# Optimization experiments

Hardware: AMD Instinct MI355X
Metric: run time of the kernel (lower is better)

The kernel has to match this reference:

```python
import jax, jax.numpy as jnp
import numpy as np

B, N, H, W = 2, 65536, 256, 256
FEA, OUT, CMP, MAX_PT = 8, 512, 32, 64
EPS = 1e-5


def _xavier(key, fan_in, fan_out):
    scale = np.sqrt(2.0 / (fan_in + fan_out)).astype(np.float32)
    return jax.random.normal(key, (fan_in, fan_out), dtype=jnp.float32) * scale


def setup_inputs() -> dict:
    key = jax.random.key(0)
    ks = jax.random.split(key, 8)
    pt_fea = jax.random.normal(ks[0], (B, N, FEA), dtype=jnp.float32)
    xy_ind = jax.random.randint(ks[1], (B, N, 2), 0, H, dtype=jnp.int32)
    return {
        "pt_fea": pt_fea,
        "bn0_g": jnp.ones((FEA,), jnp.float32), "bn0_b": jnp.zeros((FEA,), jnp.float32),
        "W1": _xavier(ks[2], FEA, 64),
        "bn1_g": jnp.ones((64,), jnp.float32), "bn1_b": jnp.zeros((64,), jnp.float32),
        "W2": _xavier(ks[3], 64, 128),
        "bn2_g": jnp.ones((128,), jnp.float32), "bn2_b": jnp.zeros((128,), jnp.float32),
        "W3": _xavier(ks[4], 128, 256),
        "bn3_g": jnp.ones((256,), jnp.float32), "bn3_b": jnp.zeros((256,), jnp.float32),
        "W4": _xavier(ks[5], 256, OUT),
        "Wc": _xavier(ks[6], OUT, CMP),
        "xy_ind": xy_ind,
    }


def _forward(pt_fea, bn0_g, bn0_b, W1, bn1_g, bn1_b, W2, bn2_g, bn2_b,
             W3, bn3_g, bn3_b, W4, Wc, xy_ind):
    Bc, Nc, Fc = pt_fea.shape
    P = Bc * Nc
    feats = pt_fea.reshape(P, Fc)
    batch_id = jnp.repeat(jnp.arange(Bc, dtype=jnp.int32), Nc)
    xy = xy_ind.reshape(P, 2)
    keys = batch_id * (H * W) + xy[:, 0] * W + xy[:, 1]  # linearized voxel id

    # random shuffle of points (torch.randperm)
    perm = jax.random.permutation(jax.random.key(42), P)
    feats = feats[perm]
    keys = keys[perm]

    # rank of each point within its voxel, in shuffled order
    # (== grp_range_torch(unq_cnt)[argsort(argsort(unq_inv))])
    order = jnp.argsort(keys)  # stable
    sk = keys[order]
    pos = jnp.arange(P)
    new_grp = jnp.concatenate([jnp.array([True]), sk[1:] != sk[:-1]])
    grp_start = jax.lax.cummax(jnp.where(new_grp, pos, 0))
    rank = jnp.zeros(P, jnp.int32).at[order].set((pos - grp_start).astype(jnp.int32))
    mask = rank < MAX_PT  # keep at most MAX_PT points per voxel

    # PPmodel: BN -> Lin -> BN -> ReLU x3 -> Lin, BN stats over kept points only
    m = mask[:, None].astype(feats.dtype)
    cnt = jnp.sum(m)

    def bn(x, g, b):
        mu = jnp.sum(x * m, axis=0) / cnt
        var = jnp.sum(jnp.square(x - mu) * m, axis=0) / cnt  # biased var
        return (x - mu) * jax.lax.rsqrt(var + EPS) * g + b

    x = bn(feats, bn0_g, bn0_b)
    x = jax.nn.relu(bn(x @ W1, bn1_g, bn1_b))
    x = jax.nn.relu(bn(x @ W2, bn2_g, bn2_b))
    x = jax.nn.relu(bn(x @ W3, bn3_g, bn3_b))
    x = x @ W4  # [P, OUT]

    # scatter_max segment reduction into dense voxel grid
    NEG = jnp.finfo(x.dtype).min
    x = jnp.where(mask[:, None], x, NEG)
    S = Bc * H * W
    pooled = jax.ops.segment_max(x, keys, num_segments=S)
    occupied = jax.ops.segment_sum(jnp.ones(P, x.dtype), keys, num_segments=S) > 0
    pooled = jnp.where(occupied[:, None], pooled, 0.0)

    comp = jax.nn.relu(pooled @ Wc)  # fea_compression
    comp = jnp.where(occupied[:, None], comp, 0.0)  # empty voxels stay zero
    out = comp.reshape(Bc, H, W, CMP).transpose(0, 3, 1, 2)  # [B, C, H, W]
    return out


def reference(pt_fea, bn0_g, bn0_b, W1, bn1_g, bn1_b, W2, bn2_g, bn2_b,
              W3, bn3_g, bn3_b, W4, Wc, xy_ind):
    return _forward(pt_fea, bn0_g, bn0_b, W1, bn1_g, bn1_b, W2, bn2_g, bn2_b,
                    W3, bn3_g, bn3_b, W4, Wc, xy_ind)
```

## Files before the change

kernel.cpp:

```cpp
#include <hip/hip_runtime.h>
#include <cstdint>
#include <cstddef>


#define P_TOT  131072
#define HWSZ   65536
#define WGRID  256
#define S_TOT  131072
#define EPS    1e-5f
#define CNTF   131072.0f

#define OFF_Y3    0ull
#define OFF_Y1    67108864ull
#define OFF_Y2    100663296ull
#define OFF_POOL  67108864ull
#define OFF_CNT   201326592ull
#define OFF_ST    201850880ull
#define OFF_OFFS  201916416ull
#define OFF_CUR   202440704ull
#define OFF_BSUM  202964992ull
#define OFF_PIDF  202969088ull
#define OFF_SEND  203493376ull
#define OFF_SKEY  204017664ull
#define OFF_W3F   204541952ull
#define OFF_W4F   204607488ull
#define OFF_WCF   204869632ull
#define OFF_W2F   204902400ull
#define OFF_SCSH  204918784ull

typedef __attribute__((ext_vector_type(8)))  short bf16x8;
typedef __attribute__((ext_vector_type(16))) float f32x16;

__device__ __forceinline__ unsigned f2bf(float f) {
    unsigned u = __float_as_uint(f);
    return (u + 0x7FFFu + ((u >> 16) & 1u)) >> 16;
}
__device__ __forceinline__ float bf2f(unsigned h) {
    return __uint_as_float(h << 16);
}

__global__ __launch_bounds__(256) void k_zero(uint4* __restrict__ p, int n_u4) {
    int i = blockIdx.x * blockDim.x + threadIdx.x;
    if (i < n_u4) p[i] = make_uint4(0u, 0u, 0u, 0u);
}

__global__ __launch_bounds__(256) void k_prepw(
    const float* __restrict__ W2, const float* __restrict__ W3,
    const float* __restrict__ W4, const float* __restrict__ Wc,
    uint4* __restrict__ W2F, uint4* __restrict__ W3F,
    uint4* __restrict__ W4F, uint4* __restrict__ WcF)
{
    int gw = (blockIdx.x * 256 + threadIdx.x) >> 6;
    int l = threadIdx.x & 63;
    const float* W; uint4* dst; int M, mt, ks, fi;
    if (gw < 64)       { fi = gw;       W = W3; dst = W3F; M = 256; mt = fi >> 3; ks = fi & 7;  }
    else if (gw < 320) { fi = gw - 64;  W = W4; dst = W4F; M = 512; mt = fi >> 4; ks = fi & 15; }
    else if (gw < 352) { fi = gw - 320; W = Wc; dst = WcF; M = 32;  mt = 0;      ks = fi;      }
    else               { fi = gw - 352; W = W2; dst = W2F; M = 128; mt = fi >> 2; ks = fi & 3;  }
    int m = mt * 32 + (l & 31);
    int k0 = ks * 16 + (l >> 5) * 8;
    unsigned p[4];
    #pragma unroll
    for (int jj = 0; jj < 4; ++jj) {
        unsigned lo = f2bf(W[(size_t)(k0 + 2*jj)     * M + m]);
        unsigned hi = f2bf(W[(size_t)(k0 + 2*jj + 1) * M + m]);
        p[jj] = lo | (hi << 16);
    }
    dst[(size_t)fi * 64 + l] = make_uint4(p[0], p[1], p[2], p[3]);
}

__global__ __launch_bounds__(256) void k_bnprep(
    const float* __restrict__ st, const float* __restrict__ g,
    const float* __restrict__ b, float* __restrict__ sc,
    float* __restrict__ sh, int nch)
{
    int c = blockIdx.x * 256 + threadIdx.x;
    if (c >= nch) return;
    float mu = st[c * 16] * (1.0f / CNTF);
    float var = st[(nch + c) * 16] * (1.0f / CNTF) - mu * mu;
    float rs = rsqrtf(var + EPS);
    float s = rs * g[c];
    sc[c] = s;
    sh[c] = b[c] - mu * s;
}

__global__ __launch_bounds__(256) void k_fold(
    unsigned short* __restrict__ y, const float* __restrict__ sc,
    const float* __restrict__ sh, int nch, int n_u4)
{
    int i = blockIdx.x * 256 + threadIdx.x;
    if (i >= n_u4) return;
    int ch0 = (i * 8) & (nch - 1);
    float4 s0 = *(const float4*)(sc + ch0), s1 = *(const float4*)(sc + ch0 + 4);
    float4 h0 = *(const float4*)(sh + ch0), h1 = *(const float4*)(sh + ch0 + 4);
    float scv[8] = {s0.x,s0.y,s0.z,s0.w,s1.x,s1.y,s1.z,s1.w};
    float shv[8] = {h0.x,h0.y,h0.z,h0.w,h1.x,h1.y,h1.z,h1.w};
    uint4 e = ((const uint4*)y)[i];
    unsigned eu[4] = {e.x, e.y, e.z, e.w};
    unsigned ou[4];
    #pragma unroll
    for (int jj = 0; jj < 4; ++jj) {
        float x0 = fmaxf(fmaf(bf2f(eu[jj] & 0xFFFFu), scv[2*jj],   shv[2*jj]),   0.f);
        float x1 = fmaxf(fmaf(bf2f(eu[jj] >> 16),     scv[2*jj+1], shv[2*jj+1]), 0.f);
        ou[jj] = f2bf(x0) | (f2bf(x1) << 16);
    }
    ((uint4*)y)[i] = make_uint4(ou[0], ou[1], ou[2], ou[3]);
}

__global__ __launch_bounds__(256) void k_stats0(
    const float* __restrict__ pt, const int* __restrict__ xy,
    float* __restrict__ st0, unsigned* __restrict__ counts)
{
    __shared__ float part[4][16];
    const int tid = threadIdx.x;
    const int p = blockIdx.x * 256 + tid;
    const float4* f4 = (const float4*)(pt + (size_t)p * 8);
    float4 a = f4[0], b = f4[1];
    float v[8] = {a.x,a.y,a.z,a.w,b.x,b.y,b.z,b.w};
    int key = (p >> 16) * HWSZ + xy[2*p] * WGRID + xy[2*p + 1];
    atomicAdd(&counts[key], 1u);
    float s[8], q[8];
    #pragma unroll
    for (int k = 0; k < 8; ++k) { s[k] = v[k]; q[k] = v[k]*v[k]; }
    #pragma unroll
    for (int k = 0; k < 8; ++k) {
        #pragma unroll
        for (int off = 32; off > 0; off >>= 1) {
            s[k] += __shfl_down(s[k], off);
            q[k] += __shfl_down(q[k], off);
        }
    }
    if ((tid & 63) == 0) {
        int w = tid >> 6;
        #pragma unroll
        for (int k = 0; k < 8; ++k) { part[w][k] = s[k]; part[w][8 + k] = q[k]; }
    }
    __syncthreads();
    if (tid < 16) {
        float t = part[0][tid] + part[1][tid] + part[2][tid] + part[3][tid];
        atomicAdd(&st0[tid * 16], t);
    }
}

__global__ __launch_bounds__(256) void k_lin1(
    const float* __restrict__ pt, const float* __restrict__ g0,
    const float* __restrict__ b0, const float* __restrict__ W1,
    const float* __restrict__ st0, float* __restrict__ y1,
    float* __restrict__ st1)
{
    __shared__ float x0s[64 * 8];
    __shared__ float w1s[8 * 64];
    __shared__ float sc0s[8], sh0s[8];
    __shared__ float red[256];
    const int tid = threadIdx.x;

    if (tid < 8) {
        float mu = st0[tid * 16] * (1.0f / CNTF);
        float var = st0[(8 + tid) * 16] * (1.0f / CNTF) - mu * mu;
        float rs = rsqrtf(var + EPS);
        sc0s[tid] = rs * g0[tid];
        sh0s[tid] = b0[tid] - mu * rs * g0[tid];
    }
    if (tid < 128) ((float4*)w1s)[tid] = ((const float4*)W1)[tid];
    const int c = tid & 63;
    const int psub = tid >> 6;
    float ssum = 0.f, ssq = 0.f;
    for (int t = 0; t < 4; ++t) {
        const int pbase = blockIdx.x * 256 + t * 64;
        __syncthreads();
        if (tid < 128) {
            float4 f = ((const float4*)(pt + (size_t)pbase * 8))[tid];
            int cc = (tid & 1) * 4;
            f.x = fmaf(f.x, sc0s[cc + 0], sh0s[cc + 0]);
            f.y = fmaf(f.y, sc0s[cc + 1], sh0s[cc + 1]);
            f.z = fmaf(f.z, sc0s[cc + 2], sh0s[cc + 2]);
            f.w = fmaf(f.w, sc0s[cc + 3], sh0s[cc + 3]);
            ((float4*)x0s)[tid] = f;
        }
        __syncthreads();
        #pragma unroll
        for (int i = 0; i < 16; ++i) {
            int pl = psub * 16 + i;
            float acc = 0.f;
            #pragma unroll
            for (int k = 0; k < 8; ++k)
                acc = fmaf(x0s[pl * 8 + k], w1s[k * 64 + c], acc);
            y1[(size_t)(pbase + pl) * 64 + c] = acc;
            ssum += acc; ssq += acc * acc;
        }
    }
    red[tid] = ssum; __syncthreads();
    if (tid < 64) atomicAdd(&st1[tid * 16],
        red[tid] + red[tid+64] + red[tid+128] + red[tid+192]);
    __syncthreads();
    red[tid] = ssq; __syncthreads();
    if (tid < 64) atomicAdd(&st1[(64 + tid) * 16],
        red[tid] + red[tid+64] + red[tid+128] + red[tid+192]);
}

__global__ __launch_bounds__(256) void k_scan1(
    const unsigned* __restrict__ counts, unsigned* __restrict__ bsum)
{
    __shared__ unsigned sh[256];
    int t = threadIdx.x;
    sh[t] = counts[blockIdx.x * 256 + t];
    __syncthreads();
    for (int d = 128; d > 0; d >>= 1) {
        if (t < d) sh[t] += sh[t + d];
        __syncthreads();
    }
    if (t == 0) bsum[blockIdx.x] = sh[0];
}

__global__ __launch_bounds__(256) void k_scan2(
    const unsigned* __restrict__ bsum, unsigned* __restrict__ boff)
{
    __shared__ unsigned sh[256];
    int t = threadIdx.x;
    unsigned a = bsum[2*t], b = bsum[2*t+1];
    unsigned s = a + b;
    sh[t] = s; __syncthreads();
    for (int d = 1; d < 256; d <<= 1) {
        unsigned u = (t >= d) ? sh[t-d] : 0u;
        __syncthreads();
        sh[t] += u;
        __syncthreads();
    }
    unsigned excl = sh[t] - s;
    boff[2*t]   = excl;
    boff[2*t+1] = excl + a;
}

__global__ __launch_bounds__(256) void k_scan3(
    const unsigned* __restrict__ counts, const unsigned* __restrict__ boff,
    unsigned* __restrict__ offs)
{
    __shared__ unsigned sh[256];
    int t = threadIdx.x, b = blockIdx.x;
    unsigned v = counts[b*256 + t];
    sh[t] = v; __syncthreads();
    for (int d = 1; d < 256; d <<= 1) {
        unsigned u = (t >= d) ? sh[t-d] : 0u;
        __syncthreads();
        sh[t] += u;
        __syncthreads();
    }
    offs[b*256 + t] = boff[b] + sh[t] - v;
}

__global__ __launch_bounds__(256) void k_fill(
    const int* __restrict__ xy, const unsigned* __restrict__ offs,
    const unsigned* __restrict__ counts, unsigned* __restrict__ cur,
    unsigned* __restrict__ pidf, unsigned* __restrict__ send,
    unsigned* __restrict__ skey)
{
    int p = blockIdx.x * 256 + threadIdx.x;
    int key = (p >> 16) * HWSZ + xy[2*p] * WGRID + xy[2*p + 1];
    unsigned o = offs[key];
    unsigned r = atomicAdd(&cur[key], 1u);
    unsigned slot = o + r;
    pidf[slot] = (unsigned)p | (r == 0 ? 0x80000000u : 0u);
    send[slot] = o + counts[key];
    skey[slot] = (unsigned)key;
}

__global__ __launch_bounds__(256, 2) void k_lin2(
    const float* __restrict__ y1, const float* __restrict__ g1,
    const float* __restrict__ b1, const uint4* __restrict__ W2F,
    const float* __restrict__ st1, unsigned short* __restrict__ y2,
    float* __restrict__ st2)
{
    __shared__ uint4 w2s[1024];
    __shared__ float sc1s[64], sh1s[64];
    const int tid = threadIdx.x, l = tid & 63, w = tid >> 6;
    if (tid < 64) {
        float mu = st1[tid * 16] * (1.0f / CNTF);
        float var = st1[(64 + tid) * 16] * (1.0f / CNTF) - mu * mu;
        float rs = rsqrtf(var + EPS);
        sc1s[tid] = rs * g1[tid];
        sh1s[tid] = b1[tid] - mu * rs * g1[tid];
    }
    #pragma unroll
    for (int r = 0; r < 4; ++r) w2s[r * 256 + tid] = W2F[r * 256 + tid];
    __syncthreads();
    const int n = l & 31, q = l >> 5;
    float s_acc[16], q_acc[16];
    #pragma unroll
    for (int r = 0; r < 16; ++r) { s_acc[r] = 0.f; q_acc[r] = 0.f; }

    for (int t = 0; t < 8; ++t) {
        const int p = (blockIdx.x * 8 + t) * 32 + n;
        const float* yrow = y1 + (size_t)p * 64 + q * 8;
        bf16x8 Bf[4];
        #pragma unroll
        for (int ks = 0; ks < 4; ++ks) {
            float4 v0 = *(const float4*)(yrow + ks * 16);
            float4 v1 = *(const float4*)(yrow + ks * 16 + 4);
            int k0 = ks * 16 + q * 8;
            float e[8] = {v0.x,v0.y,v0.z,v0.w,v1.x,v1.y,v1.z,v1.w};
            union { bf16x8 v; unsigned u[4]; } cv;
            #pragma unroll
            for (int jj = 0; jj < 4; ++jj) {
                float a0 = fmaxf(fmaf(e[2*jj],   sc1s[k0+2*jj],   sh1s[k0+2*jj]),   0.f);
                float a1 = fmaxf(fmaf(e[2*jj+1], sc1s[k0+2*jj+1], sh1s[k0+2*jj+1]), 0.f);
                cv.u[jj] = f2bf(a0) | (f2bf(a1) << 16);
            }
            Bf[ks] = cv.v;
        }
        f32x16 acc;
        #pragma unroll
        for (int r = 0; r < 16; ++r) acc[r] = 0.f;
        #pragma unroll
        for (int ks = 0; ks < 4; ++ks) {
            union { uint4 u; bf16x8 v; } av;
            av.u = w2s[(w * 4 + ks) * 64 + l];
            acc = __builtin_amdgcn_mfma_f32_32x32x16_bf16(av.v, Bf[ks], acc, 0, 0, 0);
        }
        #pragma unroll
        for (int g = 0; g < 4; ++g) {
            int ch0 = w * 32 + 8 * g + 4 * q;
            ushort4 pk;
            pk.x = (unsigned short)f2bf(acc[4*g+0]);
            pk.y = (unsigned short)f2bf(acc[4*g+1]);
            pk.z = (unsigned short)f2bf(acc[4*g+2]);
            pk.w = (unsigned short)f2bf(acc[4*g+3]);
            *(ushort4*)(y2 + (size_t)p * 128 + ch0) = pk;
        }
        #pragma unroll
        for (int r = 0; r < 16; ++r) { s_acc[r] += acc[r]; q_acc[r] += acc[r]*acc[r]; }
    }
    #pragma unroll
    for (int r = 0; r < 16; ++r) {
        float s = s_acc[r], sq = q_acc[r];
        #pragma unroll
        for (int off = 16; off > 0; off >>= 1) {
            s  += __shfl_xor(s, off);
            sq += __shfl_xor(sq, off);
        }
        if ((l & 31) == 0) {
            int ch = w * 32 + (r & 3) + 8 * (r >> 2) + 4 * q;
            atomicAdd(&st2[ch * 16], s);
            atomicAdd(&st2[(128 + ch) * 16], sq);
        }
    }
}

__global__ __launch_bounds__(256, 2) void k_lin3(
    const unsigned short* __restrict__ y2f, const uint4* __restrict__ W3F,
    unsigned short* __restrict__ y3, float* __restrict__ st3)
{
    __shared__ uint4 w3s[4096];
    const int tid = threadIdx.x, l = tid & 63, w = tid >> 6;
    #pragma unroll
    for (int r = 0; r < 16; ++r) w3s[r * 256 + tid] = W3F[r * 256 + tid];
    __syncthreads();
    const int n = l & 31, q = l >> 5;
    float s_acc[32], q_acc[32];
    #pragma unroll
    for (int r = 0; r < 32; ++r) { s_acc[r] = 0.f; q_acc[r] = 0.f; }

    for (int t = 0; t < 8; ++t) {
        const int p = (blockIdx.x * 8 + t) * 32 + n;
        const unsigned short* yrow = y2f + (size_t)p * 128 + q * 8;
        bf16x8 Bf[8];
        #pragma unroll
        for (int ks = 0; ks < 8; ++ks) {
            union { uint4 u; bf16x8 v; } bv;
            bv.u = *(const uint4*)(yrow + ks * 16);
            Bf[ks] = bv.v;
        }
        f32x16 acc[2];
        #pragma unroll
        for (int i = 0; i < 2; ++i)
            #pragma unroll
            for (int r = 0; r < 16; ++r) acc[i][r] = 0.f;
        #pragma unroll
        for (int ks = 0; ks < 8; ++ks) {
            #pragma unroll
            for (int i = 0; i < 2; ++i) {
                union { uint4 u; bf16x8 v; } av;
                av.u = w3s[((w * 2 + i) * 8 + ks) * 64 + l];
                acc[i] = __builtin_amdgcn_mfma_f32_32x32x16_bf16(av.v, Bf[ks], acc[i], 0, 0, 0);
            }
        }
        #pragma unroll
        for (int i = 0; i < 2; ++i) {
            #pragma unroll
            for (int g = 0; g < 4; ++g) {
                int ch0 = (w * 2 + i) * 32 + 8 * g + 4 * q;
                ushort4 pk;
                pk.x = (unsigned short)f2bf(acc[i][4*g+0]);
                pk.y = (unsigned short)f2bf(acc[i][4*g+1]);
                pk.z = (unsigned short)f2bf(acc[i][4*g+2]);
                pk.w = (unsigned short)f2bf(acc[i][4*g+3]);
                *(ushort4*)(y3 + (size_t)p * 256 + ch0) = pk;
            }
            #pragma unroll
            for (int r = 0; r < 16; ++r) {
                s_acc[i*16+r] += acc[i][r];
                q_acc[i*16+r] += acc[i][r] * acc[i][r];
            }
        }
    }
    #pragma unroll
    for (int i = 0; i < 2; ++i)
        #pragma unroll
        for (int r = 0; r < 16; ++r) {
            float s = s_acc[i*16+r], sq = q_acc[i*16+r];
            #pragma unroll
            for (int off = 16; off > 0; off >>= 1) {
                s  += __shfl_xor(s, off);
                sq += __shfl_xor(sq, off);
            }
            if ((l & 31) == 0) {
                int ch = (w * 2 + i) * 32 + (r & 3) + 8 * (r >> 2) + 4 * q;
                atomicAdd(&st3[ch * 16], s);
                atomicAdd(&st3[(256 + ch) * 16], sq);
            }
        }
}

__global__ __launch_bounds__(256, 2) void k_smax(
    const unsigned short* __restrict__ y3f, const uint4* __restrict__ W4F,
    const unsigned* __restrict__ pidf, const unsigned* __restrict__ send,
    const unsigned* __restrict__ skey, unsigned short* __restrict__ pooled)
{
    __shared__ float s0c_s[4 * 256];
    const int tid = threadIdx.x, l = tid & 63, w = tid >> 6;
    const int wg = blockIdx.x;
    const int q = l >> 5;

    #pragma unroll
    for (int sub = 0; sub < 4; ++sub) s0c_s[sub * 256 + tid] = -3.4e38f;

    #pragma unroll 1
    for (int t = 8; t >= 0; --t) {
        const int p0 = (wg * 8 + t) * 32;
        const int pos = p0 + (l & 31);
        const int sp = pos < P_TOT ? pos : P_TOT - 1;
        const unsigned pf = pidf[sp];
        const unsigned e_l = send[sp];
        const unsigned key_l = skey[sp];
        const unsigned cmask =
            (unsigned)__ballot((unsigned)(pos + 1) < e_l);
        const unsigned fmask =
            (unsigned)__ballot((pf & 0x80000000u) != 0u);
        const unsigned short* row =
            y3f + (size_t)(pf & 0x7FFFFFFFu) * 256 + q * 8;
        uint4 Xf[16];
        #pragma unroll
        for (int ks = 0; ks < 16; ++ks)
            Xf[ks] = *(const uint4*)(row + ks * 16);

        #pragma unroll 1
        for (int sub = 0; sub < 4; ++sub) {
            const int nt = sub * 4 + w;
            f32x16 acc;
            #pragma unroll
            for (int r = 0; r < 16; ++r) acc[r] = 0.f;
            #pragma unroll
            for (int ks = 0; ks < 16; ++ks) {
                union { uint4 u; bf16x8 v; } xv, wv;
                xv.u = Xf[ks];
                wv.u = W4F[(size_t)(nt * 16 + ks) * 64 + l];
                acc = __builtin_amdgcn_mfma_f32_32x32x16_bf16(xv.v, wv.v, acc, 0, 0, 0);
            }
            float v[32];
            #pragma unroll
            for (int r = 0; r < 16; ++r) {
                int base = (r & 3) + 8 * (r >> 2);
                float o = __shfl_xor(acc[r], 32);
                v[base]     = q ? o : acc[r];
                v[base + 4] = q ? acc[r] : o;
            }
            if ((cmask >> 31) & 1)
                v[31] = fmaxf(v[31], s0c_s[sub * 256 + tid]);
            #pragma unroll
            for (int m = 30; m >= 0; --m)
                if ((cmask >> m) & 1) v[m] = fmaxf(v[m], v[m + 1]);
            s0c_s[sub * 256 + tid] = v[0];
            if (t < 8) {
                #pragma unroll
                for (int m = 0; m < 32; ++m) {
                    if ((fmask >> m) & 1) {
                        unsigned km = (unsigned)
                            __builtin_amdgcn_readlane((int)key_l, m);
                        if ((m >> 4) == q)
                            pooled[(size_t)km * 512 + nt * 32 + (l & 31)] =
                                (unsigned short)f2bf(v[m]);
                    }
                }
            }
        }
    }
}

__global__ __launch_bounds__(256, 4) void k_out(
    const unsigned short* __restrict__ pooled, const unsigned* __restrict__ counts,
    const uint4* __restrict__ WcF, float* __restrict__ out)
{
    __shared__ uint4 wcs[2048];
    const int tid = threadIdx.x, l = tid & 63, w = tid >> 6;
    const int sbase = blockIdx.x * 128;
    #pragma unroll
    for (int r = 0; r < 8; ++r) wcs[r * 256 + tid] = WcF[r * 256 + tid];
    __syncthreads();
    const int n = l & 31, q = l >> 5;
    const int s = sbase + w * 32 + n;
    const bool occ = counts[s] > 0;
    const unsigned short* prow =
        pooled + (occ ? (size_t)s * 512 : (size_t)0) + q * 8;
    f32x16 acc;
    #pragma unroll
    for (int r = 0; r < 16; ++r) acc[r] = 0.f;

    for (int ks = 0; ks < 32; ++ks) {
        union { uint4 u; bf16x8 v; } bv;
        bv.u = *(const uint4*)(prow + ks * 16);
        union { uint4 u; bf16x8 v; } av;
        av.u = wcs[ks * 64 + l];
        acc = __builtin_amdgcn_mfma_f32_32x32x16_bf16(av.v, bv.v, acc, 0, 0, 0);
    }
    const int b = s >> 16, hw = s & 65535;
    #pragma unroll
    for (int r = 0; r < 16; ++r) {
        int ch = (r & 3) + 8 * (r >> 2) + 4 * q;
        float x = occ ? fmaxf(acc[r], 0.f) : 0.f;
        out[(size_t)b * (32 * HWSZ) + (size_t)ch * HWSZ + hw] = x;
    }
}

extern "C" void kernel_launch(void* const* d_in, const int* in_sizes, int n_in,
                              void* d_out, int out_size, void* d_ws, size_t ws_size,
                              hipStream_t stream) {
    const float* pt = (const float*)d_in[0];
    const float* g0 = (const float*)d_in[1];
    const float* b0 = (const float*)d_in[2];
    const float* W1 = (const float*)d_in[3];
    const float* g1 = (const float*)d_in[4];
    const float* b1 = (const float*)d_in[5];
    const float* W2 = (const float*)d_in[6];
    const float* g2 = (const float*)d_in[7];
    const float* b2 = (const float*)d_in[8];
    const float* W3 = (const float*)d_in[9];
    const float* g3 = (const float*)d_in[10];
    const float* b3 = (const float*)d_in[11];
    const float* W4 = (const float*)d_in[12];
    const float* Wc = (const float*)d_in[13];
    const int*   xy = (const int*)d_in[14];
    float* out = (float*)d_out;

    char* ws = (char*)d_ws;
    unsigned short* y3     = (unsigned short*)(ws + OFF_Y3);
    float*          y1     = (float*)(ws + OFF_Y1);
    unsigned short* y2     = (unsigned short*)(ws + OFF_Y2);
    unsigned short* pool16 = (unsigned short*)(ws + OFF_POOL);
    unsigned*       counts = (unsigned*)(ws + OFF_CNT);
    float*          st     = (float*)(ws + OFF_ST);
    unsigned*       offs   = (unsigned*)(ws + OFF_OFFS);
    unsigned*       cur    = (unsigned*)(ws + OFF_CUR);
    unsigned*       bsum   = (unsigned*)(ws + OFF_BSUM);
    unsigned*       pidf   = (unsigned*)(ws + OFF_PIDF);
    unsigned*       send   = (unsigned*)(ws + OFF_SEND);
    unsigned*       skey   = (unsigned*)(ws + OFF_SKEY);
    uint4* W3F = (uint4*)(ws + OFF_W3F);
    uint4* W4F = (uint4*)(ws + OFF_W4F);
    uint4* WcF = (uint4*)(ws + OFF_WCF);
    uint4* W2F = (uint4*)(ws + OFF_W2F);
    float* scsh = (float*)(ws + OFF_SCSH);
    float* sc2 = scsh;       float* sh2 = scsh + 128;
    float* sc3 = scsh + 256; float* sh3 = scsh + 512;
    float* st0 = st;
    float* st1 = st + 256;
    float* st2 = st + 2304;
    float* st3 = st + 6400;

    k_zero<<<400, 256, 0, stream>>>((uint4*)(ws + OFF_CNT), 102400);
    k_prepw<<<92, 256, 0, stream>>>(W2, W3, W4, Wc, W2F, W3F, W4F, WcF);

    k_stats0<<<512, 256, 0, stream>>>(pt, xy, st0, counts);
    k_scan1<<<512, 256, 0, stream>>>(counts, bsum);
    k_scan2<<<1,   256, 0, stream>>>(bsum, bsum + 512);
    k_scan3<<<512, 256, 0, stream>>>(counts, bsum + 512, offs);
    k_fill<<<512, 256, 0, stream>>>(xy, offs, counts, cur, pidf, send, skey);

    k_lin1<<<512, 256, 0, stream>>>(pt, g0, b0, W1, st0, y1, st1);
    k_lin2<<<512, 256, 0, stream>>>(y1, g1, b1, W2F, st1, y2, st2);
    k_bnprep<<<1, 256, 0, stream>>>(st2, g2, b2, sc2, sh2, 128);
    k_fold<<<8192, 256, 0, stream>>>(y2, sc2, sh2, 128, 2097152);
    k_lin3<<<512, 256, 0, stream>>>(y2, W3F, y3, st3);
    k_bnprep<<<1, 256, 0, stream>>>(st3, g3, b3, sc3, sh3, 256);
    k_fold<<<16384, 256, 0, stream>>>(y3, sc3, sh3, 256, 4194304);

    k_smax<<<512, 256, 0, stream>>>(y3, W4F, pidf, send, skey, pool16);
    k_out<<<S_TOT / 128, 256, 0, stream>>>(pool16, counts, WcF, out);
}
```

Measured before the change: 441.1 us.

## Fuse layer-2 BN/ReLU into lin3 loads and double smax grid

Removes the separate bnprep and fold kernels for layer 2. k_lin3 now computes the BN scale and shift from the accumulated statistics into shared memory, then applies BN and ReLU to the raw y2 values as it loads them into MFMA operands. This saves a full read and write pass over y2 and two launches, at the cost of extra ALU work per load. Separately, k_smax now gives each workgroup 4 tiles instead of 8 and launches 1024 workgroups, trading more overlap-tile recompute for more parallelism.

```diff
diff --git a/kernel.cpp b/kernel.cpp
--- a/kernel.cpp
+++ b/kernel.cpp
@@ -346,11 +346,21 @@
 }
 
 __global__ __launch_bounds__(256, 2) void k_lin3(
-    const unsigned short* __restrict__ y2f, const uint4* __restrict__ W3F,
-    unsigned short* __restrict__ y3, float* __restrict__ st3)
+    const unsigned short* __restrict__ y2raw, const float* __restrict__ g2,
+    const float* __restrict__ b2, const uint4* __restrict__ W3F,
+    const float* __restrict__ st2, unsigned short* __restrict__ y3,
+    float* __restrict__ st3)
 {
     __shared__ uint4 w3s[4096];
+    __shared__ float sc2s[128], sh2s[128];
     const int tid = threadIdx.x, l = tid & 63, w = tid >> 6;
+    if (tid < 128) {
+        float mu = st2[tid * 16] * (1.0f / CNTF);
+        float var = st2[(128 + tid) * 16] * (1.0f / CNTF) - mu * mu;
+        float rs = rsqrtf(var + EPS);
+        sc2s[tid] = rs * g2[tid];
+        sh2s[tid] = b2[tid] - mu * rs * g2[tid];
+    }
     #pragma unroll
     for (int r = 0; r < 16; ++r) w3s[r * 256 + tid] = W3F[r * 256 + tid];
     __syncthreads();
@@ -361,13 +371,23 @@
 
     for (int t = 0; t < 8; ++t) {
         const int p = (blockIdx.x * 8 + t) * 32 + n;
-        const unsigned short* yrow = y2f + (size_t)p * 128 + q * 8;
+        const unsigned short* yrow = y2raw + (size_t)p * 128 + q * 8;
         bf16x8 Bf[8];
         #pragma unroll
         for (int ks = 0; ks < 8; ++ks) {
-            union { uint4 u; bf16x8 v; } bv;
-            bv.u = *(const uint4*)(yrow + ks * 16);
-            Bf[ks] = bv.v;
+            uint4 e = *(const uint4*)(yrow + ks * 16);
+            int k0 = ks * 16 + q * 8;
+            unsigned eu[4] = {e.x, e.y, e.z, e.w};
+            union { bf16x8 v; unsigned u[4]; } cv;
+            #pragma unroll
+            for (int jj = 0; jj < 4; ++jj) {
+                float a0 = fmaxf(fmaf(bf2f(eu[jj] & 0xFFFFu),
+                                      sc2s[k0+2*jj],   sh2s[k0+2*jj]),   0.f);
+                float a1 = fmaxf(fmaf(bf2f(eu[jj] >> 16),
+                                      sc2s[k0+2*jj+1], sh2s[k0+2*jj+1]), 0.f);
+                cv.u[jj] = f2bf(a0) | (f2bf(a1) << 16);
+            }
+            Bf[ks] = cv.v;
         }
         f32x16 acc[2];
         #pragma unroll
@@ -434,8 +454,8 @@
     for (int sub = 0; sub < 4; ++sub) s0c_s[sub * 256 + tid] = -3.4e38f;
 
     #pragma unroll 1
-    for (int t = 8; t >= 0; --t) {
-        const int p0 = (wg * 8 + t) * 32;
+    for (int t = 4; t >= 0; --t) {
+        const int p0 = (wg * 4 + t) * 32;
         const int pos = p0 + (l & 31);
         const int sp = pos < P_TOT ? pos : P_TOT - 1;
         const unsigned pf = pidf[sp];
@@ -479,7 +499,7 @@
             for (int m = 30; m >= 0; --m)
                 if ((cmask >> m) & 1) v[m] = fmaxf(v[m], v[m + 1]);
             s0c_s[sub * 256 + tid] = v[0];
-            if (t < 8) {
+            if (t < 4) {
                 #pragma unroll
                 for (int m = 0; m < 32; ++m) {
                     if ((fmask >> m) & 1) {
@@ -568,8 +588,7 @@
     uint4* WcF = (uint4*)(ws + OFF_WCF);
     uint4* W2F = (uint4*)(ws + OFF_W2F);
     float* scsh = (float*)(ws + OFF_SCSH);
-    float* sc2 = scsh;       float* sh2 = scsh + 128;
-    float* sc3 = scsh + 256; float* sh3 = scsh + 512;
+    float* sc3 = scsh;       float* sh3 = scsh + 256;
     float* st0 = st;
     float* st1 = st + 256;
     float* st2 = st + 2304;
@@ -586,12 +605,10 @@
 
     k_lin1<<<512, 256, 0, stream>>>(pt, g0, b0, W1, st0, y1, st1);
     k_lin2<<<512, 256, 0, stream>>>(y1, g1, b1, W2F, st1, y2, st2);
-    k_bnprep<<<1, 256, 0, stream>>>(st2, g2, b2, sc2, sh2, 128);
-    k_fold<<<8192, 256, 0, stream>>>(y2, sc2, sh2, 128, 2097152);
-    k_lin3<<<512, 256, 0, stream>>>(y2, W3F, y3, st3);
+    k_lin3<<<512, 256, 0, stream>>>(y2, g2, b2, W3F, st2, y3, st3);
     k_bnprep<<<1, 256, 0, stream>>>(st3, g3, b3, sc3, sh3, 256);
     k_fold<<<16384, 256, 0, stream>>>(y3, sc3, sh3, 256, 4194304);
 
-    k_smax<<<512, 256, 0, stream>>>(y3, W4F, pidf, send, skey, pool16);
+    k_smax<<<1024, 256, 0, stream>>>(y3, W4F, pidf, send, skey, pool16);
     k_out<<<S_TOT / 128, 256, 0, stream>>>(pool16, counts, WcF, out);
 }
```

Result: slower. 456.1 us (+3.4%).
